# Kernel optimization log

Measured on AMD Instinct MI355X. Metric: run time of the kernel, lower is better.

Reference implementation:

```python
import jax, jax.numpy as jnp
import numpy as np

K = 7          # kernel_size
GC = 16        # group_channels (hardcoded in module)
EPS = 1e-5     # BatchNorm eps


def setup_inputs() -> dict:
    key = jax.random.key(0)
    ks = jax.random.split(key, 4)
    B, C, H, W = 4, 256, 56, 56
    Cr = C // 4                      # reduction_ratio = 4
    G = C // GC                      # groups = 16
    return {
        "x": jax.random.normal(ks[0], (B, C, H, W), jnp.float32),
        "conv1_w": jax.random.normal(ks[1], (Cr, C), jnp.float32) * 0.05,
        "bn_gamma": jnp.ones((Cr,), jnp.float32),
        "bn_beta": jnp.zeros((Cr,), jnp.float32),
        "bn_mean": jnp.zeros((Cr,), jnp.float32),
        "bn_var": jnp.ones((Cr,), jnp.float32),
        "conv2_w": jax.random.normal(ks[2], (K * K * G, Cr), jnp.float32) * 0.05,
        "conv2_b": jax.random.normal(ks[3], (K * K * G,), jnp.float32) * 0.05,
    }


def _unfold(x, k):
    # torch nn.Unfold with padding=(k-1)//2, stride=1 -> [B, C, k*k, H, W]
    B, C, H, W = x.shape
    p = (k - 1) // 2
    xp = jnp.pad(x, ((0, 0), (0, 0), (p, p), (p, p)))
    patches = jnp.stack(
        [xp[:, :, i:i + H, j:j + W] for i in range(k) for j in range(k)],
        axis=2,
    )  # (kh, kw) flattened, channel-slowest -> matches torch unfold layout
    return patches


def reference(x, conv1_w, bn_gamma, bn_beta, bn_mean, bn_var, conv2_w, conv2_b):
    B, C, H, W = x.shape
    G = C // GC
    # kernel-generation branch (stride == 1, no avgpool)
    w = jnp.einsum('bchw,oc->bohw', x, conv1_w)                 # conv1 1x1
    inv_std = jax.lax.rsqrt(bn_var + EPS)
    w = (w - bn_mean[None, :, None, None]) * (bn_gamma * inv_std)[None, :, None, None] \
        + bn_beta[None, :, None, None]                           # BN (eval)
    w = jax.nn.relu(w)
    w = jnp.einsum('bchw,oc->bohw', w, conv2_w) + conv2_b[None, :, None, None]
    w = w.reshape(B, G, K * K, H, W)                             # [B,G,K2,H,W]
    # unfold + weighted reduce
    patches = _unfold(x, K).reshape(B, G, GC, K * K, H, W)       # [B,G,gc,K2,H,W]
    out = jnp.einsum('bgkhw,bgckhw->bgchw', w, patches)          # sum over K2
    return out.reshape(B, C, H, W)
```

## Files before the change

kernel.cpp:

```cpp
#include <hip/hip_runtime.h>


#define EPS 1e-5f

typedef __fp16 half2t __attribute__((ext_vector_type(2)));
typedef __fp16 half4t __attribute__((ext_vector_type(4)));
typedef __fp16 half8t __attribute__((ext_vector_type(8)));
typedef float floatx4 __attribute__((ext_vector_type(4)));

__device__ inline half8t pack8(float4 u0, float4 u1, float s) {
    half8t a;
    half2t q;
    q = __builtin_amdgcn_cvt_pkrtz(u0.x * s, u0.y * s); a[0] = q[0]; a[1] = q[1];
    q = __builtin_amdgcn_cvt_pkrtz(u0.z * s, u0.w * s); a[2] = q[0]; a[3] = q[1];
    q = __builtin_amdgcn_cvt_pkrtz(u1.x * s, u1.y * s); a[4] = q[0]; a[5] = q[1];
    q = __builtin_amdgcn_cvt_pkrtz(u1.z * s, u1.w * s); a[6] = q[0]; a[7] = q[1];
    return a;
}

__global__ __launch_bounds__(256, 2) void k_fused(
    const float* __restrict__ x, const float* __restrict__ w1,
    const float* __restrict__ gamma, const float* __restrict__ beta,
    const float* __restrict__ mean, const float* __restrict__ var,
    const float* __restrict__ cw, const float* __restrict__ cb,
    float* __restrict__ out)
{
    __shared__ __align__(16) unsigned char smem[31760];
    __fp16* bufA = (__fp16*)smem;
    __fp16* lxh  = (__fp16*)smem;
    __fp16* lmid = (__fp16*)(smem + 9216);
    float*  lw2  = (float*)(smem + 18432);

    const int t = threadIdx.x;
    const int id  = blockIdx.x;
    const int xcd = id & 7, lid = id >> 3;
    const int wg  = (xcd < 4 ? xcd * 25 : 100 + (xcd - 4) * 24) + lid;
    const int b    = wg / 49;
    const int tile = wg % 49;
    const int th = tile / 7, tw = tile % 7;
    const int h0 = th * 8, w0 = tw * 8;
    const int lane = t & 63, wvid = t >> 6;
    const int mrow = lane & 15, quad = lane >> 4;

    const int orow = wvid * 16 + mrow;
    const float s1 = gamma[orow] * rsqrtf(var[orow] + EPS);

    half8t A[4][2];
#pragma unroll
    for (int ch = 0; ch < 4; ++ch)
#pragma unroll
        for (int h = 0; h < 2; ++h) {
            const float* src = &w1[orow * 256 + ch * 64 + h * 32 + quad * 8];
            A[ch][h] = pack8(*(const float4*)src, *(const float4*)(src + 4), s1);
        }

    const int c2 = t & 31, px8 = t >> 5;
    const float* xbase = &x[(size_t)(b * 256 + 2 * c2) * 3136 + (h0 + px8) * 56 + w0];

    float4 ca0 = *(const float4*)xbase;
    float4 ca1 = *(const float4*)(xbase + 4);
    float4 cb0 = *(const float4*)(xbase + 3136);
    float4 cb1 = *(const float4*)(xbase + 3140);

    floatx4 acc1[4] = {};
#pragma unroll
    for (int ch = 0; ch < 4; ++ch) {
        float4 na0, na1, nb0, nb1;
        if (ch < 3) {
            const float* rn = xbase + (size_t)(ch + 1) * 64 * 3136;
            na0 = *(const float4*)rn;
            na1 = *(const float4*)(rn + 4);
            nb0 = *(const float4*)(rn + 3136);
            nb1 = *(const float4*)(rn + 3140);
        }
        float fa[8], fb[8];
        fa[0]=ca0.x; fa[1]=ca0.y; fa[2]=ca0.z; fa[3]=ca0.w;
        fa[4]=ca1.x; fa[5]=ca1.y; fa[6]=ca1.z; fa[7]=ca1.w;
        fb[0]=cb0.x; fb[1]=cb0.y; fb[2]=cb0.z; fb[3]=cb0.w;
        fb[4]=cb1.x; fb[5]=cb1.y; fb[6]=cb1.z; fb[7]=cb1.w;
#pragma unroll
        for (int j = 0; j < 8; ++j) {
            half2t q = __builtin_amdgcn_cvt_pkrtz(fa[j], fb[j]);
            *(half2t*)&bufA[(px8 * 8 + j) * 72 + 2 * c2] = q;
        }
        __syncthreads();
#pragma unroll
        for (int pt = 0; pt < 4; ++pt) {
            half8t bf0 = *(const half8t*)&bufA[(pt * 16 + mrow) * 72 + quad * 8];
            half8t bf1 = *(const half8t*)&bufA[(pt * 16 + mrow) * 72 + quad * 8 + 32];
            acc1[pt] = __builtin_amdgcn_mfma_f32_16x16x32_f16(A[ch][0], bf0, acc1[pt], 0, 0, 0);
            acc1[pt] = __builtin_amdgcn_mfma_f32_16x16x32_f16(A[ch][1], bf1, acc1[pt], 0, 0, 0);
        }
        __syncthreads();
        ca0 = na0; ca1 = na1; cb0 = nb0; cb1 = nb1;
    }

    {
        float bb[4];
#pragma unroll
        for (int i = 0; i < 4; ++i) {
            int o = wvid * 16 + quad * 4 + i;
            float so = gamma[o] * rsqrtf(var[o] + EPS);
            bb[i] = beta[o] - mean[o] * so;
        }
#pragma unroll
        for (int pt = 0; pt < 4; ++pt)
#pragma unroll
            for (int i = 0; i < 4; ++i) {
                float v = fmaxf(acc1[pt][i] + bb[i], 0.f);
                lmid[(pt * 16 + mrow) * 72 + wvid * 16 + quad * 4 + i] = (__fp16)v;
            }
    }
    __syncthreads();

    const int krow = wvid * 16 + mrow;
    float4 rv4[4];
    int    rslot[4];
#pragma unroll
    for (int i = 0; i < 4; ++i) {
        int s = t + i * 256;
        rslot[i] = s;
        float4 v = make_float4(0.f, 0.f, 0.f, 0.f);
        if (s < 896) {
            int chh = s / 56, r = s % 56;
            int row = r >> 2, q = r & 3;
            int gh = h0 + row - 3;
            int gwb = w0 - 4 + q * 4;
            bool ok = (gh >= 0) & (gh < 56) & (gwb >= 0) & (gwb <= 52);
            int ghc = min(max(gh, 0), 55);
            int gwc = min(max(gwb, 0), 52);
            float4 ld = *(const float4*)&x[(size_t)(b * 256 + chh) * 3136 +
                                           ghc * 56 + gwc];
            if (ok) v = ld;
        }
        rv4[i] = v;
    }
    float4 rcw0 = make_float4(0,0,0,0), rcw1 = rcw0, rcw2 = rcw0, rcw3 = rcw0;
    if (krow < 49) {
        const float* src = &cw[(size_t)krow * 64 + quad * 8];
        rcw0 = *(const float4*)src;       rcw1 = *(const float4*)(src + 4);
        rcw2 = *(const float4*)(src + 32); rcw3 = *(const float4*)(src + 36);
    }

#pragma unroll 1
    for (int g = 0; g < 16; ++g) {
        half8t a0 = pack8(rcw0, rcw1, 1.f);
        half8t a1 = pack8(rcw2, rcw3, 1.f);
        if (krow >= 49) { a0 = half8t{}; a1 = half8t{}; }

        {
            float bias[4];
            int   kor[4];
#pragma unroll
            for (int i = 0; i < 4; ++i) {
                kor[i]  = wvid * 16 + quad * 4 + i;
                bias[i] = (kor[i] < 49) ? cb[g * 49 + kor[i]] : 0.f;
            }
#pragma unroll
            for (int pt = 0; pt < 4; ++pt) {
                half8t b0 = *(const half8t*)&lmid[(pt * 16 + mrow) * 72 + quad * 8];
                half8t b1 = *(const half8t*)&lmid[(pt * 16 + mrow) * 72 + quad * 8 + 32];
                floatx4 acc = {0.f, 0.f, 0.f, 0.f};
                acc = __builtin_amdgcn_mfma_f32_16x16x32_f16(a0, b0, acc, 0, 0, 0);
                acc = __builtin_amdgcn_mfma_f32_16x16x32_f16(a1, b1, acc, 0, 0, 0);
#pragma unroll
                for (int i = 0; i < 4; ++i)
                    if (kor[i] < 49)
                        lw2[kor[i] * 68 + pt * 16 + mrow] = acc[i] + bias[i];
            }
        }

#pragma unroll
        for (int i = 0; i < 4; ++i) {
            int s = rslot[i];
            if (s < 896) {
                int chh = s / 56, r = s % 56;
                int row = r >> 2, q = r & 3;
                half2t p0 = __builtin_amdgcn_cvt_pkrtz(rv4[i].x, rv4[i].y);
                half2t p1 = __builtin_amdgcn_cvt_pkrtz(rv4[i].z, rv4[i].w);
                half4t h; h[0] = p0[0]; h[1] = p0[1]; h[2] = p1[0]; h[3] = p1[1];
                *(half4t*)&lxh[chh * 280 + row * 20 + q * 4] = h;
            }
        }

        if (g < 15) {
#pragma unroll
            for (int i = 0; i < 4; ++i) {
                int s = rslot[i];
                float4 v = make_float4(0.f, 0.f, 0.f, 0.f);
                if (s < 896) {
                    int chh = s / 56, r = s % 56;
                    int row = r >> 2, q = r & 3;
                    int gh = h0 + row - 3;
                    int gwb = w0 - 4 + q * 4;
                    bool ok = (gh >= 0) & (gh < 56) & (gwb >= 0) & (gwb <= 52);
                    int ghc = min(max(gh, 0), 55);
                    int gwc = min(max(gwb, 0), 52);
                    float4 ld = *(const float4*)&x[(size_t)(b * 256 + (g + 1) * 16 + chh) * 3136 +
                                                   ghc * 56 + gwc];
                    if (ok) v = ld;
                }
                rv4[i] = v;
            }
            if (krow < 49) {
                const float* src = &cw[(size_t)((g + 1) * 49 + krow) * 64 + quad * 8];
                rcw0 = *(const float4*)src;        rcw1 = *(const float4*)(src + 4);
                rcw2 = *(const float4*)(src + 32); rcw3 = *(const float4*)(src + 36);
            }
        }
        __syncthreads();

        {
            const int cc = t >> 4, pxt = t & 15;
            const int sh = pxt >> 1, sw4 = (pxt & 1) * 4;
            float a0f = 0.f, a1f = 0.f, a2f = 0.f, a3f = 0.f;
#pragma unroll
            for (int kh = 0; kh < 7; ++kh) {
                const int rbh = cc * 280 + (sh + kh) * 20 + sw4;
                half4t f0 = *(const half4t*)&lxh[rbh];
                half4t f1 = *(const half4t*)&lxh[rbh + 4];
                half4t f2 = *(const half4t*)&lxh[rbh + 8];
                float xw[12];
#pragma unroll
                for (int j = 0; j < 4; ++j) {
                    xw[j]     = (float)f0[j];
                    xw[j + 4] = (float)f1[j];
                    xw[j + 8] = (float)f2[j];
                }
#pragma unroll
                for (int kw = 0; kw < 7; ++kw) {
                    const float4 wv = *(const float4*)&lw2[(kh * 7 + kw) * 68 + pxt * 4];
                    a0f = fmaf(wv.x, xw[kw + 1], a0f);
                    a1f = fmaf(wv.y, xw[kw + 2], a1f);
                    a2f = fmaf(wv.z, xw[kw + 3], a2f);
                    a3f = fmaf(wv.w, xw[kw + 4], a3f);
                }
            }
            *(float4*)&out[(size_t)(b * 256 + g * 16 + cc) * 3136 +
                           (h0 + sh) * 56 + w0 + sw4] =
                make_float4(a0f, a1f, a2f, a3f);
        }
        __syncthreads();
    }
}

extern "C" void kernel_launch(void* const* d_in, const int* in_sizes, int n_in,
                              void* d_out, int out_size, void* d_ws, size_t ws_size,
                              hipStream_t stream) {
    const float* x     = (const float*)d_in[0];
    const float* w1    = (const float*)d_in[1];
    const float* gamma = (const float*)d_in[2];
    const float* beta  = (const float*)d_in[3];
    const float* mean  = (const float*)d_in[4];
    const float* var   = (const float*)d_in[5];
    const float* cw    = (const float*)d_in[6];
    const float* cb    = (const float*)d_in[7];
    float* out = (float*)d_out;

    (void)d_ws; (void)ws_size;

    k_fused<<<dim3(196), 256, 0, stream>>>(x, w1, gamma, beta, mean, var,
                                           cw, cb, out);
}
```

Before: 114.8 us.

## Double block size and split groups and pixel tiles across two thread halves

Launches 512 threads per block. The conv1 MFMA work is split so each wave handles half of the pixel tiles, and the group loop is divided between two 256-thread halves that process alternating groups with separate LDS buffers. This is meant to raise per-CU parallelism, since the grid has fewer blocks than CUs, and to halve the serial group loop length. In exchange it uses more LDS and raises register pressure under the 512-thread launch bound.

```diff
diff --git a/kernel.cpp b/kernel.cpp
--- a/kernel.cpp
+++ b/kernel.cpp
@@ -18,18 +18,16 @@
     return a;
 }
 
-__global__ __launch_bounds__(256, 2) void k_fused(
+__global__ __launch_bounds__(512, 2) void k_fused(
     const float* __restrict__ x, const float* __restrict__ w1,
     const float* __restrict__ gamma, const float* __restrict__ beta,
     const float* __restrict__ mean, const float* __restrict__ var,
     const float* __restrict__ cw, const float* __restrict__ cb,
     float* __restrict__ out)
 {
-    __shared__ __align__(16) unsigned char smem[31760];
+    __shared__ __align__(16) unsigned char smem[54048];
     __fp16* bufA = (__fp16*)smem;
-    __fp16* lxh  = (__fp16*)smem;
     __fp16* lmid = (__fp16*)(smem + 9216);
-    float*  lw2  = (float*)(smem + 18432);
 
     const int t = threadIdx.x;
     const int id  = blockIdx.x;
@@ -42,7 +40,8 @@
     const int lane = t & 63, wvid = t >> 6;
     const int mrow = lane & 15, quad = lane >> 4;
 
-    const int orow = wvid * 16 + mrow;
+    const int ow = wvid & 3, ph = wvid >> 2;
+    const int orow = ow * 16 + mrow;
     const float s1 = gamma[orow] * rsqrtf(var[orow] + EPS);
 
     half8t A[4][2];
@@ -54,71 +53,73 @@
             A[ch][h] = pack8(*(const float4*)src, *(const float4*)(src + 4), s1);
         }
 
-    const int c2 = t & 31, px8 = t >> 5;
-    const float* xbase = &x[(size_t)(b * 256 + 2 * c2) * 3136 + (h0 + px8) * 56 + w0];
-
-    float4 ca0 = *(const float4*)xbase;
-    float4 ca1 = *(const float4*)(xbase + 4);
-    float4 cb0 = *(const float4*)(xbase + 3136);
-    float4 cb1 = *(const float4*)(xbase + 3140);
-
-    floatx4 acc1[4] = {};
+    const int c2 = t & 31, pq = t >> 5;
+    const int srow = pq >> 1, ch4 = (pq & 1) * 4;
+    const float* xbase = &x[(size_t)(b * 256 + 2 * c2) * 3136 +
+                            (h0 + srow) * 56 + w0 + ch4];
+
+    float4 ca = *(const float4*)xbase;
+    float4 cbv = *(const float4*)(xbase + 3136);
+
+    floatx4 acc1[2] = {};
 #pragma unroll
     for (int ch = 0; ch < 4; ++ch) {
-        float4 na0, na1, nb0, nb1;
+        float4 na, nb;
         if (ch < 3) {
             const float* rn = xbase + (size_t)(ch + 1) * 64 * 3136;
-            na0 = *(const float4*)rn;
-            na1 = *(const float4*)(rn + 4);
-            nb0 = *(const float4*)(rn + 3136);
-            nb1 = *(const float4*)(rn + 3140);
-        }
-        float fa[8], fb[8];
-        fa[0]=ca0.x; fa[1]=ca0.y; fa[2]=ca0.z; fa[3]=ca0.w;
-        fa[4]=ca1.x; fa[5]=ca1.y; fa[6]=ca1.z; fa[7]=ca1.w;
-        fb[0]=cb0.x; fb[1]=cb0.y; fb[2]=cb0.z; fb[3]=cb0.w;
-        fb[4]=cb1.x; fb[5]=cb1.y; fb[6]=cb1.z; fb[7]=cb1.w;
-#pragma unroll
-        for (int j = 0; j < 8; ++j) {
+            na = *(const float4*)rn;
+            nb = *(const float4*)(rn + 3136);
+        }
+        const float* fa = (const float*)&ca;
+        const float* fb = (const float*)&cbv;
+#pragma unroll
+        for (int j = 0; j < 4; ++j) {
             half2t q = __builtin_amdgcn_cvt_pkrtz(fa[j], fb[j]);
-            *(half2t*)&bufA[(px8 * 8 + j) * 72 + 2 * c2] = q;
-        }
-        __syncthreads();
-#pragma unroll
-        for (int pt = 0; pt < 4; ++pt) {
+            *(half2t*)&bufA[(srow * 8 + ch4 + j) * 72 + 2 * c2] = q;
+        }
+        __syncthreads();
+#pragma unroll
+        for (int p2 = 0; p2 < 2; ++p2) {
+            int pt = ph * 2 + p2;
             half8t bf0 = *(const half8t*)&bufA[(pt * 16 + mrow) * 72 + quad * 8];
             half8t bf1 = *(const half8t*)&bufA[(pt * 16 + mrow) * 72 + quad * 8 + 32];
-            acc1[pt] = __builtin_amdgcn_mfma_f32_16x16x32_f16(A[ch][0], bf0, acc1[pt], 0, 0, 0);
-            acc1[pt] = __builtin_amdgcn_mfma_f32_16x16x32_f16(A[ch][1], bf1, acc1[pt], 0, 0, 0);
-        }
-        __syncthreads();
-        ca0 = na0; ca1 = na1; cb0 = nb0; cb1 = nb1;
+            acc1[p2] = __builtin_amdgcn_mfma_f32_16x16x32_f16(A[ch][0], bf0, acc1[p2], 0, 0, 0);
+            acc1[p2] = __builtin_amdgcn_mfma_f32_16x16x32_f16(A[ch][1], bf1, acc1[p2], 0, 0, 0);
+        }
+        __syncthreads();
+        ca = na; cbv = nb;
     }
 
     {
         float bb[4];
 #pragma unroll
         for (int i = 0; i < 4; ++i) {
-            int o = wvid * 16 + quad * 4 + i;
+            int o = ow * 16 + quad * 4 + i;
             float so = gamma[o] * rsqrtf(var[o] + EPS);
             bb[i] = beta[o] - mean[o] * so;
         }
 #pragma unroll
-        for (int pt = 0; pt < 4; ++pt)
+        for (int p2 = 0; p2 < 2; ++p2)
 #pragma unroll
             for (int i = 0; i < 4; ++i) {
-                float v = fmaxf(acc1[pt][i] + bb[i], 0.f);
-                lmid[(pt * 16 + mrow) * 72 + wvid * 16 + quad * 4 + i] = (__fp16)v;
+                float v = fmaxf(acc1[p2][i] + bb[i], 0.f);
+                lmid[((ph * 2 + p2) * 16 + mrow) * 72 + ow * 16 + quad * 4 + i] = (__fp16)v;
             }
     }
     __syncthreads();
 
-    const int krow = wvid * 16 + mrow;
+    const int hs = wvid >> 2;
+    const int wl = wvid & 3;
+    const int tl = t & 255;
+    __fp16* myxh = (hs == 0) ? (__fp16*)smem : (__fp16*)(smem + 45088);
+    float*  mylw = (float*)(smem + 18432 + hs * 13328);
+    const int krow = wl * 16 + mrow;
+
     float4 rv4[4];
     int    rslot[4];
 #pragma unroll
     for (int i = 0; i < 4; ++i) {
-        int s = t + i * 256;
+        int s = tl + i * 256;
         rslot[i] = s;
         float4 v = make_float4(0.f, 0.f, 0.f, 0.f);
         if (s < 896) {
@@ -129,7 +130,7 @@
             bool ok = (gh >= 0) & (gh < 56) & (gwb >= 0) & (gwb <= 52);
             int ghc = min(max(gh, 0), 55);
             int gwc = min(max(gwb, 0), 52);
-            float4 ld = *(const float4*)&x[(size_t)(b * 256 + chh) * 3136 +
+            float4 ld = *(const float4*)&x[(size_t)(b * 256 + hs * 16 + chh) * 3136 +
                                            ghc * 56 + gwc];
             if (ok) v = ld;
         }
@@ -137,13 +138,15 @@
     }
     float4 rcw0 = make_float4(0,0,0,0), rcw1 = rcw0, rcw2 = rcw0, rcw3 = rcw0;
     if (krow < 49) {
-        const float* src = &cw[(size_t)krow * 64 + quad * 8];
-        rcw0 = *(const float4*)src;       rcw1 = *(const float4*)(src + 4);
+        const float* src = &cw[(size_t)(hs * 49 + krow) * 64 + quad * 8];
+        rcw0 = *(const float4*)src;        rcw1 = *(const float4*)(src + 4);
         rcw2 = *(const float4*)(src + 32); rcw3 = *(const float4*)(src + 36);
     }
 
 #pragma unroll 1
-    for (int g = 0; g < 16; ++g) {
+    for (int gi = 0; gi < 8; ++gi) {
+        const int g = gi * 2 + hs;
+
         half8t a0 = pack8(rcw0, rcw1, 1.f);
         half8t a1 = pack8(rcw2, rcw3, 1.f);
         if (krow >= 49) { a0 = half8t{}; a1 = half8t{}; }
@@ -153,7 +156,7 @@
             int   kor[4];
 #pragma unroll
             for (int i = 0; i < 4; ++i) {
-                kor[i]  = wvid * 16 + quad * 4 + i;
+                kor[i]  = wl * 16 + quad * 4 + i;
                 bias[i] = (kor[i] < 49) ? cb[g * 49 + kor[i]] : 0.f;
             }
 #pragma unroll
@@ -166,7 +169,7 @@
 #pragma unroll
                 for (int i = 0; i < 4; ++i)
                     if (kor[i] < 49)
-                        lw2[kor[i] * 68 + pt * 16 + mrow] = acc[i] + bias[i];
+                        mylw[kor[i] * 68 + pt * 16 + mrow] = acc[i] + bias[i];
             }
         }
 
@@ -178,12 +181,12 @@
                 int row = r >> 2, q = r & 3;
                 half2t p0 = __builtin_amdgcn_cvt_pkrtz(rv4[i].x, rv4[i].y);
                 half2t p1 = __builtin_amdgcn_cvt_pkrtz(rv4[i].z, rv4[i].w);
-                half4t h; h[0] = p0[0]; h[1] = p0[1]; h[2] = p1[0]; h[3] = p1[1];
-                *(half4t*)&lxh[chh * 280 + row * 20 + q * 4] = h;
-            }
-        }
-
-        if (g < 15) {
+                half4t hv; hv[0] = p0[0]; hv[1] = p0[1]; hv[2] = p1[0]; hv[3] = p1[1];
+                *(half4t*)&myxh[chh * 280 + row * 20 + q * 4] = hv;
+            }
+        }
+
+        if (gi < 7) {
 #pragma unroll
             for (int i = 0; i < 4; ++i) {
                 int s = rslot[i];
@@ -196,14 +199,14 @@
                     bool ok = (gh >= 0) & (gh < 56) & (gwb >= 0) & (gwb <= 52);
                     int ghc = min(max(gh, 0), 55);
                     int gwc = min(max(gwb, 0), 52);
-                    float4 ld = *(const float4*)&x[(size_t)(b * 256 + (g + 1) * 16 + chh) * 3136 +
+                    float4 ld = *(const float4*)&x[(size_t)(b * 256 + (g + 2) * 16 + chh) * 3136 +
                                                    ghc * 56 + gwc];
                     if (ok) v = ld;
                 }
                 rv4[i] = v;
             }
             if (krow < 49) {
-                const float* src = &cw[(size_t)((g + 1) * 49 + krow) * 64 + quad * 8];
+                const float* src = &cw[(size_t)((g + 2) * 49 + krow) * 64 + quad * 8];
                 rcw0 = *(const float4*)src;        rcw1 = *(const float4*)(src + 4);
                 rcw2 = *(const float4*)(src + 32); rcw3 = *(const float4*)(src + 36);
             }
@@ -211,15 +214,15 @@
         __syncthreads();
 
         {
-            const int cc = t >> 4, pxt = t & 15;
+            const int cc = tl >> 4, pxt = tl & 15;
             const int sh = pxt >> 1, sw4 = (pxt & 1) * 4;
             float a0f = 0.f, a1f = 0.f, a2f = 0.f, a3f = 0.f;
 #pragma unroll
             for (int kh = 0; kh < 7; ++kh) {
                 const int rbh = cc * 280 + (sh + kh) * 20 + sw4;
-                half4t f0 = *(const half4t*)&lxh[rbh];
-                half4t f1 = *(const half4t*)&lxh[rbh + 4];
-                half4t f2 = *(const half4t*)&lxh[rbh + 8];
+                half4t f0 = *(const half4t*)&myxh[rbh];
+                half4t f1 = *(const half4t*)&myxh[rbh + 4];
+                half4t f2 = *(const half4t*)&myxh[rbh + 8];
                 float xw[12];
 #pragma unroll
                 for (int j = 0; j < 4; ++j) {
@@ -229,7 +232,7 @@
                 }
 #pragma unroll
                 for (int kw = 0; kw < 7; ++kw) {
-                    const float4 wv = *(const float4*)&lw2[(kh * 7 + kw) * 68 + pxt * 4];
+                    const float4 wv = *(const float4*)&mylw[(kh * 7 + kw) * 68 + pxt * 4];
                     a0f = fmaf(wv.x, xw[kw + 1], a0f);
                     a1f = fmaf(wv.y, xw[kw + 2], a1f);
                     a2f = fmaf(wv.z, xw[kw + 3], a2f);
@@ -259,6 +262,6 @@
 
     (void)d_ws; (void)ws_size;
 
-    k_fused<<<dim3(196), 256, 0, stream>>>(x, w1, gamma, beta, mean, var,
+    k_fused<<<dim3(196), 512, 0, stream>>>(x, w1, gamma, beta, mean, var,
                                            cw, cb, out);
 }
```

Result: faster. 107.2 us (-6.6%).
